# Kernel tuning notes

Measured on AMD Instinct MI355X. Metric: run time of the kernel, lower is better.

The kernel has to match this reference:

```python
import jax, jax.numpy as jnp
import numpy as np

SIGMA = 0.05  # gaussian bandwidth from the source


def _sqdist(a, b):
    # a: [B,N,D], b: [B,M,D] -> [B,N,M] squared euclidean distance
    a2 = jnp.sum(a * a, axis=-1)[:, :, None]
    b2 = jnp.sum(b * b, axis=-1)[:, None, :]
    return a2 + b2 - 2.0 * jnp.einsum('bnd,bmd->bnm', a, b)


def setup_inputs() -> dict:
    key = jax.random.key(0)
    k1, k2, k3, k4 = jax.random.split(key, 4)
    B, N, D = 2, 4096, 32
    points = jax.random.normal(k1, (B, N, 3), dtype=jnp.float32)
    pointfea1 = jax.random.normal(k2, (B, N, D), dtype=jnp.float32)
    pointfea2 = jax.random.normal(k3, (B, N, D), dtype=jnp.float32)
    weights = jax.random.uniform(k4, (B, N), dtype=jnp.float32) / N  # point-cloud mass weights
    return {"points": points, "pointfea1": pointfea1, "pointfea2": pointfea2, "weights": weights}


def reference(points, pointfea1, pointfea2, weights):
    # naive_corres: per-point spatial log-gaussian softmax vs feature log-softmax,
    # weighted squared difference, reduced over both pair axes -> [B]
    x = points / SIGMA
    point_loggauss = jax.nn.log_softmax(-_sqdist(x, x), axis=2)          # [B,N,N]
    fea_logsoftmax = jax.nn.log_softmax(-_sqdist(pointfea1, pointfea2), axis=2)  # [B,N,N]
    diff2 = (jnp.exp(point_loggauss) - jnp.exp(fea_logsoftmax)) ** 2
    l2_loss = jnp.sum(diff2 * weights[:, :, None], axis=2)  # sum over j
    return jnp.sum(l2_loss, axis=1)                          # sum over i -> [B]
```

## Files before the change

kernel.cpp:

```cpp
#include <hip/hip_runtime.h>

#define D    32
#define BLK  256
#define NCH  16
#define SJ   128

#define LOG2E 1.44269504088896340736f

typedef short  short8  __attribute__((ext_vector_type(8)));
typedef float  floatx4 __attribute__((ext_vector_type(4)));
typedef float  v2f     __attribute__((ext_vector_type(2)));

__device__ __forceinline__ short f2bf(float v) {
    union { float f; unsigned u; } x; x.f = v;
    unsigned r = x.u + 0x7fffu + ((x.u >> 16) & 1u);
    return (short)(r >> 16);
}
__device__ __forceinline__ float bf2f(short h) {
    union { float f; unsigned u; } x;
    x.u = ((unsigned)(unsigned short)h) << 16;
    return x.f;
}
__device__ __forceinline__ float fast_exp2(float x) {
#if __has_builtin(__builtin_amdgcn_exp2f)
    return __builtin_amdgcn_exp2f(x);
#else
    return exp2f(x);
#endif
}

__global__ __launch_bounds__(BLK) void precompute_kernel(
    const float* __restrict__ points,
    const float* __restrict__ fea1,
    const float* __restrict__ fea2,
    float4* __restrict__ xp,
    float* __restrict__ f1n,
    float* __restrict__ f2n,
    short* __restrict__ f2hi,
    short* __restrict__ f2lo,
    float* __restrict__ acc,
    float* __restrict__ out,
    int BN, int Bsz)
{
    int r = blockIdx.x * BLK + threadIdx.x;
    if (r < Bsz) out[r] = 0.0f;
    if (r >= BN) return;
#pragma unroll
    for (int s = 0; s < 5; ++s) acc[s * BN + r] = 0.0f;

    const float s20 = 20.0f;
    float x = points[3*r+0] * s20;
    float y = points[3*r+1] * s20;
    float z = points[3*r+2] * s20;
    float4 v; v.x = x; v.y = y; v.z = z;
    v.w = (x*x + y*y + z*z) * LOG2E;
    xp[r] = v;

    const float4* p1 = (const float4*)(fea1 + (size_t)r * D);
    float n1 = 0.f;
#pragma unroll
    for (int k = 0; k < D/4; ++k) {
        float4 a = p1[k];
        n1 = fmaf(a.x,a.x, fmaf(a.y,a.y, fmaf(a.z,a.z, fmaf(a.w,a.w, n1))));
    }
    f1n[r] = n1 * LOG2E;

    const int t = r >> 4;
    const int m = r & 15;
    const float* p2 = fea2 + (size_t)r * D;
    float n2 = 0.f;
#pragma unroll
    for (int q = 0; q < 4; ++q) {
        float4 v0 = *(const float4*)(p2 + q*8);
        float4 v1 = *(const float4*)(p2 + q*8 + 4);
        float e[8] = {v0.x,v0.y,v0.z,v0.w,v1.x,v1.y,v1.z,v1.w};
        short8 h, l;
#pragma unroll
        for (int k = 0; k < 8; ++k) {
            n2 = fmaf(e[k], e[k], n2);
            short hh = f2bf(e[k]);
            h[k] = hh;
            l[k] = f2bf(e[k] - bf2f(hh));
        }
        size_t off = ((size_t)t * 64 + m + 16*q) * 8;
        *(short8*)&f2hi[off] = h;
        *(short8*)&f2lo[off] = l;
    }
    f2n[r] = n2 * LOG2E;
}

__global__ __launch_bounds__(BLK) void pair_kernel(
    const float* __restrict__ fea1,
    const short* __restrict__ f2hi,
    const short* __restrict__ f2lo,
    const float4* __restrict__ xp,
    const float* __restrict__ f1n,
    const float* __restrict__ f2n,
    float* __restrict__ acc,
    int N, int BN)
{
    __shared__ __align__(16) short sHi[SJ * D];
    __shared__ __align__(16) short sLo[SJ * D];
    __shared__ float4 sXJ[SJ];
    __shared__ float  sFN[SJ];

    const int tid  = threadIdx.x;
    const int lane = tid & 63;
    const int wv   = tid >> 6;
    const int m    = lane & 15;
    const int q    = lane >> 4;

    const int ibpb  = N / 64;
    const int b     = blockIdx.x / ibpb;
    const int ibase = blockIdx.x * 64 + wv * 16;
    const int JCH   = N / NCH;
    const int jc0   = blockIdx.y * JCH;

    const float* f1p = fea1 + (size_t)(ibase + m) * D + q * 8;
    float4 bv0 = *(const float4*)(f1p);
    float4 bv1 = *(const float4*)(f1p + 4);
    float bf[8] = {bv0.x,bv0.y,bv0.z,bv0.w,bv1.x,bv1.y,bv1.z,bv1.w};
    short8 Bhi, Blo;
#pragma unroll
    for (int k = 0; k < 8; ++k) {
        short h = f2bf(bf[k]);
        Bhi[k] = h;
        Blo[k] = f2bf(bf[k] - bf2f(h));
    }

    const float L2 = 2.0f * LOG2E;
    float4 xi = xp[ibase + m];
    float xix = xi.x * L2, xiy = xi.y * L2, xiz = xi.z * L2;
    float mxiw = -xi.w;
    float nfi  = -f1n[ibase + m];

    v2f sAB = {0.f, 0.f};
    v2f s2  = {0.f, 0.f};
    float sab = 0.f;

    const short*  gHi  = f2hi + ((size_t)(b * N + jc0) >> 4) * 512;
    const short*  gLo  = f2lo + ((size_t)(b * N + jc0) >> 4) * 512;
    const float4* xpb  = xp  + (size_t)b * N + jc0;
    const float*  f2nb = f2n + (size_t)b * N + jc0;

    for (int s = 0; s < JCH; s += SJ) {
        const uint4* srcH = (const uint4*)(gHi + (size_t)(s >> 4) * 512);
        const uint4* srcL = (const uint4*)(gLo + (size_t)(s >> 4) * 512);
        uint4* dstH = (uint4*)sHi;
        uint4* dstL = (uint4*)sLo;
        dstH[tid]       = srcH[tid];
        dstH[tid + 256] = srcH[tid + 256];
        dstL[tid]       = srcL[tid];
        dstL[tid + 256] = srcL[tid + 256];
        if (tid < SJ) {
            sXJ[tid] = xpb[s + tid];
            sFN[tid] = f2nb[s + tid];
        }
        __syncthreads();

#pragma unroll 2
        for (int jt8 = 0; jt8 < SJ/16; ++jt8) {
            const short8 Ahi = *(const short8*)&sHi[(jt8 * 64 + lane) * 8];
            const short8 Alo = *(const short8*)&sLo[(jt8 * 64 + lane) * 8];
            floatx4 c = {0.f, 0.f, 0.f, 0.f};
            c = __builtin_amdgcn_mfma_f32_16x16x32_bf16(Ahi, Bhi, c, 0, 0, 0);
            c = __builtin_amdgcn_mfma_f32_16x16x32_bf16(Ahi, Blo, c, 0, 0, 0);
            c = __builtin_amdgcn_mfma_f32_16x16x32_bf16(Alo, Bhi, c, 0, 0, 0);
#pragma unroll
            for (int r = 0; r < 4; ++r) {
                int jl = jt8 * 16 + q * 4 + r;
                float4 xj = sXJ[jl];
                float bL = fmaf(c[r], L2, nfi - sFN[jl]);
                float aL = fmaf(xiz, xj.z,
                             fmaf(xiy, xj.y,
                              fmaf(xix, xj.x, mxiw))) - xj.w;
                float ea = fast_exp2(aL);
                float eb = fast_exp2(bL);
                v2f e = {ea, eb};
                sAB += e;
                s2   = __builtin_elementwise_fma(e, e, s2);
                sab  = fmaf(ea, eb, sab);
            }
        }
        __syncthreads();
    }

    float vA = sAB.x, vB = sAB.y, v2a = s2.x, v2b = s2.y;
    vA  += __shfl_xor(vA, 16);  vA  += __shfl_xor(vA, 32);
    vB  += __shfl_xor(vB, 16);  vB  += __shfl_xor(vB, 32);
    v2a += __shfl_xor(v2a, 16); v2a += __shfl_xor(v2a, 32);
    v2b += __shfl_xor(v2b, 16); v2b += __shfl_xor(v2b, 32);
    sab += __shfl_xor(sab, 16); sab += __shfl_xor(sab, 32);

    if (lane < 16) {
        int row = ibase + lane;
        atomicAdd(&acc[0*BN + row], vA);
        atomicAdd(&acc[1*BN + row], v2a);
        atomicAdd(&acc[2*BN + row], vB);
        atomicAdd(&acc[3*BN + row], v2b);
        atomicAdd(&acc[4*BN + row], sab);
    }
}

__global__ __launch_bounds__(BLK) void finalize_kernel(
    const float* __restrict__ acc,
    const float* __restrict__ weights,
    float* __restrict__ out,
    int N, int BN)
{
    int row = blockIdx.x * BLK + threadIdx.x;
    int b   = (blockIdx.x * BLK) / N;

    float A   = acc[0*BN + row];
    float S2a = acc[1*BN + row];
    float Bt  = acc[2*BN + row];
    float S2b = acc[3*BN + row];
    float Sab = acc[4*BN + row];
    float invA = 1.0f / A;
    float invB = 1.0f / Bt;
    float val  = S2a*invA*invA - 2.0f*Sab*invA*invB + S2b*invB*invB;
    float sum  = weights[row] * val;

    __shared__ float red[BLK/64];
    for (int off = 32; off > 0; off >>= 1)
        sum += __shfl_down(sum, off);
    if ((threadIdx.x & 63) == 0) red[threadIdx.x >> 6] = sum;
    __syncthreads();
    if (threadIdx.x == 0) {
        float s = 0.f;
#pragma unroll
        for (int w = 0; w < BLK/64; ++w) s += red[w];
        atomicAdd(&out[b], s);
    }
}

extern "C" void kernel_launch(void* const* d_in, const int* in_sizes, int n_in,
                              void* d_out, int out_size, void* d_ws, size_t ws_size,
                              hipStream_t stream) {
    const float* points  = (const float*)d_in[0];
    const float* fea1    = (const float*)d_in[1];
    const float* fea2    = (const float*)d_in[2];
    const float* weights = (const float*)d_in[3];
    float* out = (float*)d_out;

    int B  = out_size;
    int BN = in_sizes[3];
    int N  = BN / B;

    float*  acc  = (float*)d_ws;
    float4* xp   = (float4*)((char*)d_ws + (size_t)5  * BN * 4);
    float*  f2n  = (float*)((char*)d_ws + (size_t)9  * BN * 4);
    float*  f1n  = (float*)((char*)d_ws + (size_t)10 * BN * 4);
    short*  f2hi = (short*)((char*)d_ws + (size_t)11 * BN * 4);
    short*  f2lo = f2hi + (size_t)BN * D;

    precompute_kernel<<<dim3((BN + BLK - 1) / BLK), dim3(BLK), 0, stream>>>(
        points, fea1, fea2, xp, f1n, f2n, f2hi, f2lo, acc, out, BN, B);

    dim3 grid(BN / 64, NCH);
    pair_kernel<<<grid, dim3(BLK), 0, stream>>>(
        fea1, f2hi, f2lo, xp, f1n, f2n, acc, N, BN);

    finalize_kernel<<<dim3(BN / BLK), dim3(BLK), 0, stream>>>(acc, weights, out, N, BN);
}
```

Before: 86.04 us.

## Restructure pair kernel: each wave covers 64 rows, reads j tiles directly from global

The fea1 hi/lo bf16 split now happens once in the precompute kernel and is stored in MFMA-tiled layout. In the pair kernel each wave holds all 64 i-rows of the block in registers and takes its own slice of the j-chunk, loading A tiles and point data straight from global memory. This removes shared-memory staging and the __syncthreads barriers, and each j tile is reused across four MFMA row groups. The cost is more registers per thread, a 4x larger atomic reduction epilogue, and uncoalesced-ish global loads relying on cache.

Result: slower. 90.66 us (+5.4%).

```diff
diff --git a/kernel.cpp b/kernel.cpp
--- a/kernel.cpp
+++ b/kernel.cpp
@@ -3,8 +3,6 @@
 #define D    32
 #define BLK  256
 #define NCH  16
-#define SJ   128
-
 #define LOG2E 1.44269504088896340736f
 
 typedef short  short8  __attribute__((ext_vector_type(8)));
@@ -36,6 +34,8 @@
     float4* __restrict__ xp,
     float* __restrict__ f1n,
     float* __restrict__ f2n,
+    short* __restrict__ f1hi,
+    short* __restrict__ f1lo,
     short* __restrict__ f2hi,
     short* __restrict__ f2lo,
     float* __restrict__ acc,
@@ -56,41 +56,49 @@
     v.w = (x*x + y*y + z*z) * LOG2E;
     xp[r] = v;
 
-    const float4* p1 = (const float4*)(fea1 + (size_t)r * D);
-    float n1 = 0.f;
-#pragma unroll
-    for (int k = 0; k < D/4; ++k) {
-        float4 a = p1[k];
-        n1 = fmaf(a.x,a.x, fmaf(a.y,a.y, fmaf(a.z,a.z, fmaf(a.w,a.w, n1))));
-    }
-    f1n[r] = n1 * LOG2E;
-
     const int t = r >> 4;
     const int m = r & 15;
+    const float* p1 = fea1 + (size_t)r * D;
     const float* p2 = fea2 + (size_t)r * D;
-    float n2 = 0.f;
+    float n1 = 0.f, n2 = 0.f;
 #pragma unroll
     for (int q = 0; q < 4; ++q) {
-        float4 v0 = *(const float4*)(p2 + q*8);
-        float4 v1 = *(const float4*)(p2 + q*8 + 4);
-        float e[8] = {v0.x,v0.y,v0.z,v0.w,v1.x,v1.y,v1.z,v1.w};
-        short8 h, l;
+        size_t off = ((size_t)t * 64 + m + 16*q) * 8;
+        float4 a0 = *(const float4*)(p1 + q*8);
+        float4 a1 = *(const float4*)(p1 + q*8 + 4);
+        float e1[8] = {a0.x,a0.y,a0.z,a0.w,a1.x,a1.y,a1.z,a1.w};
+        short8 h1, l1;
 #pragma unroll
         for (int k = 0; k < 8; ++k) {
-            n2 = fmaf(e[k], e[k], n2);
-            short hh = f2bf(e[k]);
-            h[k] = hh;
-            l[k] = f2bf(e[k] - bf2f(hh));
-        }
-        size_t off = ((size_t)t * 64 + m + 16*q) * 8;
-        *(short8*)&f2hi[off] = h;
-        *(short8*)&f2lo[off] = l;
-    }
+            n1 = fmaf(e1[k], e1[k], n1);
+            short hh = f2bf(e1[k]);
+            h1[k] = hh;
+            l1[k] = f2bf(e1[k] - bf2f(hh));
+        }
+        *(short8*)&f1hi[off] = h1;
+        *(short8*)&f1lo[off] = l1;
+
+        float4 b0 = *(const float4*)(p2 + q*8);
+        float4 b1 = *(const float4*)(p2 + q*8 + 4);
+        float e2[8] = {b0.x,b0.y,b0.z,b0.w,b1.x,b1.y,b1.z,b1.w};
+        short8 h2, l2;
+#pragma unroll
+        for (int k = 0; k < 8; ++k) {
+            n2 = fmaf(e2[k], e2[k], n2);
+            short hh = f2bf(e2[k]);
+            h2[k] = hh;
+            l2[k] = f2bf(e2[k] - bf2f(hh));
+        }
+        *(short8*)&f2hi[off] = h2;
+        *(short8*)&f2lo[off] = l2;
+    }
+    f1n[r] = n1 * LOG2E;
     f2n[r] = n2 * LOG2E;
 }
 
 __global__ __launch_bounds__(BLK) void pair_kernel(
-    const float* __restrict__ fea1,
+    const short* __restrict__ f1hi,
+    const short* __restrict__ f1lo,
     const short* __restrict__ f2hi,
     const short* __restrict__ f2lo,
     const float4* __restrict__ xp,
@@ -99,106 +107,91 @@
     float* __restrict__ acc,
     int N, int BN)
 {
-    __shared__ __align__(16) short sHi[SJ * D];
-    __shared__ __align__(16) short sLo[SJ * D];
-    __shared__ float4 sXJ[SJ];
-    __shared__ float  sFN[SJ];
-
     const int tid  = threadIdx.x;
     const int lane = tid & 63;
     const int wv   = tid >> 6;
     const int m    = lane & 15;
     const int q    = lane >> 4;
 
-    const int ibpb  = N / 64;
+    const int ibpb  = N >> 6;
     const int b     = blockIdx.x / ibpb;
-    const int ibase = blockIdx.x * 64 + wv * 16;
+    const int ibase = blockIdx.x << 6;
     const int JCH   = N / NCH;
     const int jc0   = blockIdx.y * JCH;
 
-    const float* f1p = fea1 + (size_t)(ibase + m) * D + q * 8;
-    float4 bv0 = *(const float4*)(f1p);
-    float4 bv1 = *(const float4*)(f1p + 4);
-    float bf[8] = {bv0.x,bv0.y,bv0.z,bv0.w,bv1.x,bv1.y,bv1.z,bv1.w};
-    short8 Bhi, Blo;
-#pragma unroll
-    for (int k = 0; k < 8; ++k) {
-        short h = f2bf(bf[k]);
-        Bhi[k] = h;
-        Blo[k] = f2bf(bf[k] - bf2f(h));
-    }
-
     const float L2 = 2.0f * LOG2E;
-    float4 xi = xp[ibase + m];
-    float xix = xi.x * L2, xiy = xi.y * L2, xiz = xi.z * L2;
-    float mxiw = -xi.w;
-    float nfi  = -f1n[ibase + m];
-
-    v2f sAB = {0.f, 0.f};
-    v2f s2  = {0.f, 0.f};
-    float sab = 0.f;
-
-    const short*  gHi  = f2hi + ((size_t)(b * N + jc0) >> 4) * 512;
-    const short*  gLo  = f2lo + ((size_t)(b * N + jc0) >> 4) * 512;
-    const float4* xpb  = xp  + (size_t)b * N + jc0;
-    const float*  f2nb = f2n + (size_t)b * N + jc0;
-
-    for (int s = 0; s < JCH; s += SJ) {
-        const uint4* srcH = (const uint4*)(gHi + (size_t)(s >> 4) * 512);
-        const uint4* srcL = (const uint4*)(gLo + (size_t)(s >> 4) * 512);
-        uint4* dstH = (uint4*)sHi;
-        uint4* dstL = (uint4*)sLo;
-        dstH[tid]       = srcH[tid];
-        dstH[tid + 256] = srcH[tid + 256];
-        dstL[tid]       = srcL[tid];
-        dstL[tid + 256] = srcL[tid + 256];
-        if (tid < SJ) {
-            sXJ[tid] = xpb[s + tid];
-            sFN[tid] = f2nb[s + tid];
-        }
-        __syncthreads();
-
-#pragma unroll 2
-        for (int jt8 = 0; jt8 < SJ/16; ++jt8) {
-            const short8 Ahi = *(const short8*)&sHi[(jt8 * 64 + lane) * 8];
-            const short8 Alo = *(const short8*)&sLo[(jt8 * 64 + lane) * 8];
+
+    short8 Bh[4], Bl[4];
+    float xsx[4], xsy[4], xsz[4], mw[4], nf[4];
+#pragma unroll
+    for (int it = 0; it < 4; ++it) {
+        size_t ti = ((size_t)(blockIdx.x * 4 + it) * 64 + lane) * 8;
+        Bh[it] = *(const short8*)&f1hi[ti];
+        Bl[it] = *(const short8*)&f1lo[ti];
+        int irow = ibase + it*16 + m;
+        float4 xi = xp[irow];
+        xsx[it] = xi.x * L2; xsy[it] = xi.y * L2; xsz[it] = xi.z * L2;
+        mw[it] = -xi.w;
+        nf[it] = -f1n[irow];
+    }
+
+    v2f  sAB[4] = {{0.f,0.f},{0.f,0.f},{0.f,0.f},{0.f,0.f}};
+    v2f  s2 [4] = {{0.f,0.f},{0.f,0.f},{0.f,0.f},{0.f,0.f}};
+    float sab[4] = {0.f,0.f,0.f,0.f};
+
+    const int ntw    = JCH >> 6;
+    const int tjbase = (b * N + jc0) >> 4;
+
+    for (int t = 0; t < ntw; ++t) {
+        const int jt = wv * ntw + t;
+        const size_t tj = ((size_t)(tjbase + jt) * 64 + lane) * 8;
+        short8 Ah = *(const short8*)&f2hi[tj];
+        short8 Al = *(const short8*)&f2lo[tj];
+
+        const int jb = b * N + jc0 + jt * 16 + q * 4;
+        float4 xjv[4];
+        xjv[0] = xp[jb+0]; xjv[1] = xp[jb+1]; xjv[2] = xp[jb+2]; xjv[3] = xp[jb+3];
+        floatx4 fnr = *(const floatx4*)&f2n[jb];
+
+#pragma unroll
+        for (int it = 0; it < 4; ++it) {
             floatx4 c = {0.f, 0.f, 0.f, 0.f};
-            c = __builtin_amdgcn_mfma_f32_16x16x32_bf16(Ahi, Bhi, c, 0, 0, 0);
-            c = __builtin_amdgcn_mfma_f32_16x16x32_bf16(Ahi, Blo, c, 0, 0, 0);
-            c = __builtin_amdgcn_mfma_f32_16x16x32_bf16(Alo, Bhi, c, 0, 0, 0);
+            c = __builtin_amdgcn_mfma_f32_16x16x32_bf16(Ah, Bh[it], c, 0, 0, 0);
+            c = __builtin_amdgcn_mfma_f32_16x16x32_bf16(Ah, Bl[it], c, 0, 0, 0);
+            c = __builtin_amdgcn_mfma_f32_16x16x32_bf16(Al, Bh[it], c, 0, 0, 0);
 #pragma unroll
             for (int r = 0; r < 4; ++r) {
-                int jl = jt8 * 16 + q * 4 + r;
-                float4 xj = sXJ[jl];
-                float bL = fmaf(c[r], L2, nfi - sFN[jl]);
-                float aL = fmaf(xiz, xj.z,
-                             fmaf(xiy, xj.y,
-                              fmaf(xix, xj.x, mxiw))) - xj.w;
+                float aL = fmaf(xsz[it], xjv[r].z,
+                             fmaf(xsy[it], xjv[r].y,
+                              fmaf(xsx[it], xjv[r].x, mw[it]))) - xjv[r].w;
+                float bL = fmaf(c[r], L2, nf[it] - fnr[r]);
                 float ea = fast_exp2(aL);
                 float eb = fast_exp2(bL);
                 v2f e = {ea, eb};
-                sAB += e;
-                s2   = __builtin_elementwise_fma(e, e, s2);
-                sab  = fmaf(ea, eb, sab);
+                sAB[it] += e;
+                s2[it]   = __builtin_elementwise_fma(e, e, s2[it]);
+                sab[it]  = fmaf(ea, eb, sab[it]);
             }
         }
-        __syncthreads();
-    }
-
-    float vA = sAB.x, vB = sAB.y, v2a = s2.x, v2b = s2.y;
-    vA  += __shfl_xor(vA, 16);  vA  += __shfl_xor(vA, 32);
-    vB  += __shfl_xor(vB, 16);  vB  += __shfl_xor(vB, 32);
-    v2a += __shfl_xor(v2a, 16); v2a += __shfl_xor(v2a, 32);
-    v2b += __shfl_xor(v2b, 16); v2b += __shfl_xor(v2b, 32);
-    sab += __shfl_xor(sab, 16); sab += __shfl_xor(sab, 32);
-
-    if (lane < 16) {
-        int row = ibase + lane;
-        atomicAdd(&acc[0*BN + row], vA);
-        atomicAdd(&acc[1*BN + row], v2a);
-        atomicAdd(&acc[2*BN + row], vB);
-        atomicAdd(&acc[3*BN + row], v2b);
-        atomicAdd(&acc[4*BN + row], sab);
+    }
+
+#pragma unroll
+    for (int it = 0; it < 4; ++it) {
+        float vA = sAB[it].x, vB = sAB[it].y;
+        float v2a = s2[it].x, v2b = s2[it].y, vab = sab[it];
+        vA  += __shfl_xor(vA, 16);  vA  += __shfl_xor(vA, 32);
+        vB  += __shfl_xor(vB, 16);  vB  += __shfl_xor(vB, 32);
+        v2a += __shfl_xor(v2a, 16); v2a += __shfl_xor(v2a, 32);
+        v2b += __shfl_xor(v2b, 16); v2b += __shfl_xor(v2b, 32);
+        vab += __shfl_xor(vab, 16); vab += __shfl_xor(vab, 32);
+        if (lane < 16) {
+            int row = ibase + it*16 + lane;
+            atomicAdd(&acc[0*BN + row], vA);
+            atomicAdd(&acc[1*BN + row], v2a);
+            atomicAdd(&acc[2*BN + row], vB);
+            atomicAdd(&acc[3*BN + row], v2b);
+            atomicAdd(&acc[4*BN + row], vab);
+        }
     }
 }
 
@@ -251,15 +244,17 @@
     float4* xp   = (float4*)((char*)d_ws + (size_t)5  * BN * 4);
     float*  f2n  = (float*)((char*)d_ws + (size_t)9  * BN * 4);
     float*  f1n  = (float*)((char*)d_ws + (size_t)10 * BN * 4);
-    short*  f2hi = (short*)((char*)d_ws + (size_t)11 * BN * 4);
+    short*  f1hi = (short*)((char*)d_ws + (size_t)11 * BN * 4);
+    short*  f1lo = f1hi + (size_t)BN * D;
+    short*  f2hi = f1lo + (size_t)BN * D;
     short*  f2lo = f2hi + (size_t)BN * D;
 
     precompute_kernel<<<dim3((BN + BLK - 1) / BLK), dim3(BLK), 0, stream>>>(
-        points, fea1, fea2, xp, f1n, f2n, f2hi, f2lo, acc, out, BN, B);
+        points, fea1, fea2, xp, f1n, f2n, f1hi, f1lo, f2hi, f2lo, acc, out, BN, B);
 
     dim3 grid(BN / 64, NCH);
     pair_kernel<<<grid, dim3(BLK), 0, stream>>>(
-        fea1, f2hi, f2lo, xp, f1n, f2n, acc, N, BN);
+        f1hi, f1lo, f2hi, f2lo, xp, f1n, f2n, acc, N, BN);
 
     finalize_kernel<<<dim3(BN / BLK), dim3(BLK), 0, stream>>>(acc, weights, out, N, BN);
 }
```
